# Performance work log

Hardware: AMD Instinct MI355X
Metric: run time of the kernel (lower is better)

The kernel has to match this reference:

```python
import jax, jax.numpy as jnp
import numpy as np

B = 32768
H = 320          # pred_hidden
V = 34           # num_classes
BLANK = V - 1    # padding_idx for embedding


def setup_inputs() -> dict:
    key = jax.random.key(0)
    ks = jax.random.split(key, 12)
    s = 0.05
    embed_W = jax.random.normal(ks[0], (V, H), jnp.float32) * s
    embed_W = embed_W.at[BLANK].set(0.0)  # padding_idx row is zeros in torch
    return {
        "x": jax.random.randint(ks[1], (B,), 0, V, jnp.int32),
        "enc_proj_line": jax.random.normal(ks[2], (B, H), jnp.float32),
        "h": jax.random.normal(ks[3], (1, B, H), jnp.float32),
        "c": jax.random.normal(ks[4], (1, B, H), jnp.float32),
        "embed_W": embed_W,
        "W_ih": jax.random.normal(ks[5], (4 * H, H), jnp.float32) * s,
        "W_hh": jax.random.normal(ks[6], (4 * H, H), jnp.float32) * s,
        "b_ih": jax.random.normal(ks[7], (4 * H,), jnp.float32) * s,
        "b_hh": jax.random.normal(ks[8], (4 * H,), jnp.float32) * s,
        "pred_W": jax.random.normal(ks[9], (H, H), jnp.float32) * s,
        "pred_b": jnp.zeros((H,), jnp.float32),
        "joint_W": jax.random.normal(ks[10], (V, H), jnp.float32) * s,
        "joint_b": jnp.zeros((V,), jnp.float32),
    }


def reference(x, enc_proj_line, h, c, embed_W, W_ih, W_hh, b_ih, b_hh,
              pred_W, pred_b, joint_W, joint_b):
    # embedding lookup: [B, H]
    emb = embed_W[x]
    # single-timestep LSTM cell (torch gate order: i, f, g, o)
    gates = emb @ W_ih.T + b_ih + h[0] @ W_hh.T + b_hh  # [B, 4H]
    i, f, g, o = jnp.split(gates, 4, axis=-1)
    i = jax.nn.sigmoid(i)
    f = jax.nn.sigmoid(f)
    g = jnp.tanh(g)
    o = jax.nn.sigmoid(o)
    c_new = f * c[0] + i * g                 # [B, H]
    h_new = o * jnp.tanh(c_new)              # [B, H] == g[0] (lstm output)
    # pred projection + joint
    pred_proj = h_new @ pred_W.T + pred_b    # [B, H]
    joint_out = (enc_proj_line + pred_proj) @ joint_W.T + joint_b  # [B, V]
    dec = jnp.argmax(joint_out, axis=-1)
    return dec, h_new[None], c_new[None]
```

## Files before the change

kernel.cpp:

```cpp
#include <hip/hip_runtime.h>
#include <math.h>

#define NB 32768
#define H 320
#define V 34
#define N4 1280
#define BM 128
#define BN 128
#define BK 32
#define KSTEPS (H / BK)
#define NWG ((NB / BM) * (N4 / BN))

typedef _Float16 f16;
typedef f16 f16x4 __attribute__((ext_vector_type(4)));
typedef f16 f16x8 __attribute__((ext_vector_type(8)));
typedef float f32x4 __attribute__((ext_vector_type(4)));

#define WS_GTP 0
#define WS_JB2 54400
#define WS_B_BYTE 217744
#define BT_COUNT (N4 * H)
#define WS_JP_BYTE 1856144
#define JP_COUNT (48 * 640)
#define WS_AT_BYTE 1979136
#define AT_COUNT (NB * H)

#define JBM 64
#define JBK 32
#define JKSTEPS 20

#define PREP_P4 1280
#define PREP_P2 50
#define PREP_P0 170
#define PREP_P3 120
#define PREP_NWG (PREP_P4 + PREP_P2 + PREP_P0 + PREP_P3 + 1)

__device__ __forceinline__ float sigf(float x) {
    return 1.0f / (1.0f + __expf(-x));
}
__device__ __forceinline__ float tanh_fast(float x) {
    return 1.0f - 2.0f / (1.0f + __expf(2.0f * x));
}

typedef const __attribute__((address_space(1))) unsigned int* gas_t;
typedef __attribute__((address_space(3))) unsigned int* las_t;

__device__ __forceinline__ void split8(const float* e, f16x8& p1, f16x8& p2) {
    #pragma unroll
    for (int j = 0; j < 8; ++j) {
        f16 a = (f16)e[j];
        p1[j] = a;
        p2[j] = (f16)((e[j] - (float)a) * 2048.0f);
    }
}

__device__ __forceinline__ void split8_res(const float* e, f16x8& p1, f16x8& p2) {
    #pragma unroll
    for (int j = 0; j < 8; ++j) {
        f16 a = (f16)e[j];
        p1[j] = a;
        p2[j] = (f16)(e[j] - (float)a);
    }
}

__global__ void prep(const float* __restrict__ embed_W,
                     const float* __restrict__ W_ih,
                     const float* __restrict__ b_ih,
                     const float* __restrict__ b_hh,
                     const float* __restrict__ pred_W,
                     const float* __restrict__ pred_b,
                     const float* __restrict__ joint_W,
                     const float* __restrict__ joint_b,
                     const float* __restrict__ W_hh,
                     const float* __restrict__ h_in,
                     float* __restrict__ ws) {
    const int bid = blockIdx.x;
    const int t = threadIdx.x;
    if (bid < PREP_P4) {
        int id = bid * 256 + t;
        int ks = id >> 15, m = id & 32767;
        const float* src = h_in + (size_t)m * H + ks * 32;
        f16* at1 = (f16*)((char*)ws + WS_AT_BYTE);
        f16* at2 = at1 + AT_COUNT;
        size_t tbase = ((size_t)(m >> 7) * KSTEPS + ks) * 4096
                       + ((m & 127) >> 4) * 512 + (m & 15) * 8;
        #pragma unroll
        for (int g = 0; g < 4; ++g) {
            float4 v0 = *(const float4*)(src + g * 8);
            float4 v1 = *(const float4*)(src + g * 8 + 4);
            float e[8] = {v0.x, v0.y, v0.z, v0.w, v1.x, v1.y, v1.z, v1.w};
            f16x8 p1, p2;
            split8_res(e, p1, p2);
            *(f16x8*)(at1 + tbase + g * 128) = p1;
            *(f16x8*)(at2 + tbase + g * 128) = p2;
        }
    } else if (bid < PREP_P4 + PREP_P2) {
        int id = (bid - PREP_P4) * 256 + t;
        int ks = id / 1280, n = id - ks * 1280;
        int orig = (n & 3) * H + (n >> 2);
        const float* src = W_hh + (size_t)orig * H + ks * 32;
        f16* bt1 = (f16*)((char*)ws + WS_B_BYTE);
        f16* bt2 = bt1 + BT_COUNT;
        size_t tbase = ((size_t)(n >> 7) * KSTEPS + ks) * 4096
                       + ((n & 127) >> 4) * 512 + (n & 15) * 8;
        #pragma unroll
        for (int g = 0; g < 4; ++g) {
            float4 v0 = *(const float4*)(src + g * 8);
            float4 v1 = *(const float4*)(src + g * 8 + 4);
            float e[8] = {v0.x, v0.y, v0.z, v0.w, v1.x, v1.y, v1.z, v1.w};
            f16x8 p1, p2;
            split8(e, p1, p2);
            *(f16x8*)(bt1 + tbase + g * 128) = p1;
            *(f16x8*)(bt2 + tbase + g * 128) = p2;
        }
    } else if (bid < PREP_P4 + PREP_P2 + PREP_P0) {
        int id = (bid - PREP_P4 - PREP_P2) * 256 + t;
        int v = id / N4, n = id % N4;
        int orig = (n & 3) * H + (n >> 2);
        float acc = b_ih[orig] + b_hh[orig];
        const float* e = embed_W + (size_t)v * H;
        const float* w = W_ih + (size_t)orig * H;
        for (int k = 0; k < H; k += 4) {
            float4 e4 = *(const float4*)(e + k);
            float4 w4 = *(const float4*)(w + k);
            acc = fmaf(e4.x, w4.x, acc);
            acc = fmaf(e4.y, w4.y, acc);
            acc = fmaf(e4.z, w4.z, acc);
            acc = fmaf(e4.w, w4.w, acc);
        }
        ws[WS_GTP + id] = acc;
    } else if (bid < PREP_P4 + PREP_P2 + PREP_P0 + PREP_P3) {
        int id = (bid - PREP_P4 - PREP_P2 - PREP_P0) * 256 + t;
        int n = id / 640, k = id % 640;
        float wv = 0.0f;
        if (n < V) {
            if (k < H) {
                wv = joint_W[(size_t)n * H + k];
            } else {
                float acc = 0.0f;
                const float* jw = joint_W + (size_t)n * H;
                for (int j = 0; j < H; ++j)
                    acc = fmaf(jw[j], pred_W[(size_t)j * H + (k - H)], acc);
                wv = acc;
            }
        }
        f16 w1 = (f16)wv;
        f16 w2 = (f16)((wv - (float)w1) * 2048.0f);
        int kk = k & 31;
        int off = (k >> 5) * 1536 + (n >> 4) * 512 + (kk >> 3) * 128
                  + (n & 15) * 8 + (kk & 7);
        f16* jp1 = (f16*)((char*)ws + WS_JP_BYTE);
        jp1[off] = w1;
        jp1[JP_COUNT + off] = w2;
    } else {
        if (t < V) {
            float acc = joint_b[t];
            const float* jw = joint_W + (size_t)t * H;
            for (int j = 0; j < H; ++j)
                acc = fmaf(jw[j], pred_b[j], acc);
            ws[WS_JB2 + t] = acc;
        }
    }
}

__launch_bounds__(256, 3)
__global__ void lstm_gemm_fast(const int* __restrict__ x,
                               const float* __restrict__ c_in,
                               const float* __restrict__ ws,
                               float* __restrict__ out) {
    __shared__ __align__(16) char smem[32768];
    const int tid = threadIdx.x, lane = tid & 63, w = tid >> 6;

    int l = (blockIdx.x & 7) * (NWG / 8) + (blockIdx.x >> 3);
    const int mb = l / (N4 / BN);
    const int nb = l % (N4 / BN);
    const int m0 = mb * BM, n0 = nb * BN;

    const f16* At1 = (const f16*)((const char*)ws + WS_AT_BYTE);
    const f16* At2 = At1 + AT_COUNT;
    const f16* Bt1 = (const f16*)((const char*)ws + WS_B_BYTE);
    const f16* Bt2 = Bt1 + BT_COUNT;
    const float* gtp = ws + WS_GTP;
    float* hn_out = out + NB;
    float* cn_out = out + NB + (size_t)NB * H;

    const int asub = (w >> 1) * 4;
    const int bsub = (w & 1) * 4;
    const int lo = lane * 8;

    auto stageB = [&](int ks, int parity) {
        const f16* srcp = (w < 2) ? Bt1 : Bt2;
        const f16* src = srcp + (size_t)(nb * KSTEPS + ks) * 4096 + (w & 1) * 2048;
        char* dst = smem + parity * 16384 + (w >> 1) * 8192 + (w & 1) * 4096;
        #pragma unroll
        for (int i = 0; i < 4; ++i) {
            __builtin_amdgcn_global_load_lds(
                (gas_t)(const void*)(src + i * 512 + lane * 8),
                (las_t)(void*)(dst + i * 1024), 16, 0, 0);
        }
    };

    f32x4 acc[4][4];
    #pragma unroll
    for (int i = 0; i < 4; ++i)
        #pragma unroll
        for (int j = 0; j < 4; ++j)
            acc[i][j] = (f32x4){0.f, 0.f, 0.f, 0.f};

    f16x8 a1r[2][4], a2rr[4], b1[4], b2[4];

    stageB(0, 0);
    __builtin_amdgcn_sched_barrier(0);
    {
        const f16* a1b = At1 + (size_t)(mb * KSTEPS + 0) * 4096;
        #pragma unroll
        for (int mi = 0; mi < 4; ++mi)
            a1r[0][mi] = *(const f16x8*)(a1b + (asub + mi) * 512 + lo);
    }
    asm volatile("s_waitcnt vmcnt(4)" ::: "memory");
    __builtin_amdgcn_sched_barrier(0);
    __builtin_amdgcn_s_barrier();

    #pragma unroll
    for (int t = 0; t < KSTEPS; ++t) {
        const int cb = t & 1;
        const f16* B1 = (const f16*)(smem + cb * 16384);
        const f16* B2 = B1 + 4096;

        #pragma unroll
        for (int nj = 0; nj < 4; ++nj)
            b1[nj] = *(const f16x8*)(B1 + (bsub + nj) * 512 + lo);
        #pragma unroll
        for (int nj = 0; nj < 4; ++nj)
            b2[nj] = *(const f16x8*)(B2 + (bsub + nj) * 512 + lo);
        __builtin_amdgcn_sched_barrier(0);
        {
            const f16* a2b = At2 + (size_t)(mb * KSTEPS + t) * 4096;
            #pragma unroll
            for (int mi = 0; mi < 4; ++mi)
                a2rr[mi] = *(const f16x8*)(a2b + (asub + mi) * 512 + lo);
        }
        __builtin_amdgcn_sched_barrier(0);
        if (t < KSTEPS - 1) {
            stageB(t + 1, cb ^ 1);
            __builtin_amdgcn_sched_barrier(0);
            const f16* a1b = At1 + (size_t)(mb * KSTEPS + (t + 1)) * 4096;
            #pragma unroll
            for (int mi = 0; mi < 4; ++mi)
                a1r[cb ^ 1][mi] = *(const f16x8*)(a1b + (asub + mi) * 512 + lo);
            __builtin_amdgcn_sched_barrier(0);
        }

        __builtin_amdgcn_s_setprio(1);
        #pragma unroll
        for (int mi = 0; mi < 4; ++mi)
            #pragma unroll
            for (int nj = 0; nj < 4; ++nj)
                acc[mi][nj] = __builtin_amdgcn_mfma_f32_16x16x32_f16(
                    a1r[cb][mi], b1[nj], acc[mi][nj], 0, 0, 0);
        __builtin_amdgcn_s_setprio(0);
        #pragma unroll
        for (int mi = 0; mi < 4; ++mi)
            #pragma unroll
            for (int j = 0; j < 8; ++j)
                a1r[cb][mi][j] = a1r[cb][mi][j] * (f16)0.00048828125f;
        __builtin_amdgcn_s_setprio(1);
        #pragma unroll
        for (int mi = 0; mi < 4; ++mi)
            #pragma unroll
            for (int nj = 0; nj < 4; ++nj)
                acc[mi][nj] = __builtin_amdgcn_mfma_f32_16x16x32_f16(
                    a1r[cb][mi], b2[nj], acc[mi][nj], 0, 0, 0);
        #pragma unroll
        for (int mi = 0; mi < 4; ++mi)
            #pragma unroll
            for (int nj = 0; nj < 4; ++nj)
                acc[mi][nj] = __builtin_amdgcn_mfma_f32_16x16x32_f16(
                    a2rr[mi], b1[nj], acc[mi][nj], 0, 0, 0);
        __builtin_amdgcn_s_setprio(0);

        if (t < KSTEPS - 1) {
            asm volatile("s_waitcnt vmcnt(4)" ::: "memory");
            __builtin_amdgcn_sched_barrier(0);
            __builtin_amdgcn_s_barrier();
        } else {
            __syncthreads();
        }
    }

    const int wn = (w & 1) * 64;
    const int hk0 = n0 >> 2;
    float* gates = (float*)smem;
    #pragma unroll
    for (int hf = 0; hf < 2; ++hf) {
        if ((w >> 1) == hf) {
            #pragma unroll
            for (int mi = 0; mi < 4; ++mi)
                #pragma unroll
                for (int nj = 0; nj < 4; ++nj) {
                    f32x4 v = acc[mi][nj];
                    int n = wn + nj * 16 + (lane & 15);
                    int lr0 = mi * 16 + (lane >> 4) * 4;
                    #pragma unroll
                    for (int q = 0; q < 4; ++q) {
                        int lr = lr0 + q;
                        gates[lr * 128 + (n ^ ((lr & 7) << 2))] = v[q];
                    }
                }
        }
        __syncthreads();
        #pragma unroll 2
        for (int it = 0; it < 8; ++it) {
            int idx = it * 256 + tid;
            int ml = idx >> 5, hkl = idx & 31;
            int k0 = (ml & 7) << 2;
            f32x4 g4 = *(const f32x4*)&gates[ml * 128 + ((hkl * 4) ^ k0)];
            int m = m0 + hf * 64 + ml;
            int hk = hk0 + hkl;
            int xv = x[m];
            float4 b4 = *(const float4*)(gtp + (size_t)xv * N4 + n0 + hkl * 4);
            float ig = sigf(g4[0] + b4.x);
            float fg = sigf(g4[1] + b4.y);
            float gg = tanh_fast(g4[2] + b4.z);
            float og = sigf(g4[3] + b4.w);
            float cv = c_in[(size_t)m * H + hk];
            float cn = fmaf(fg, cv, ig * gg);
            float hn = og * tanh_fast(cn);
            hn_out[(size_t)m * H + hk] = hn;
            cn_out[(size_t)m * H + hk] = cn;
        }
        if (hf == 0) __syncthreads();
    }
}

__launch_bounds__(256, 2)
__global__ void joint_argmax(const float* __restrict__ enc,
                             const float* __restrict__ ws,
                             float* __restrict__ out) {
    __shared__ __align__(16) char smem[28672];
    const int tid = threadIdx.x, lane = tid & 63, w = tid >> 6;
    const int m0 = blockIdx.x * JBM;

    const f16* Jp1 = (const f16*)((const char*)ws + WS_JP_BYTE);
    const f16* Jp2 = Jp1 + JP_COUNT;
    const float* hn = out + NB;
    const float* jb2 = ws + WS_JB2;

    f16* base = (f16*)smem;

    f32x4 accM[3], accC[3];
    #pragma unroll
    for (int j = 0; j < 3; ++j) {
        accM[j] = (f32x4){0.f, 0.f, 0.f, 0.f};
        accC[j] = (f32x4){0.f, 0.f, 0.f, 0.f};
    }

    auto stage = [&](int t, f16* A1, f16* A2, f16* B1, f16* B2) {
        const float* srcp = (t < 10) ? enc : hn;
        const int koff = (t % 10) * JBK;
        int row = (tid >> 6) * 16 + (tid & 15);
        int k0 = ((tid & 63) >> 4) * 8;
        const float* sp = srcp + (size_t)(m0 + row) * H + koff + k0;
        float4 v0 = *(const float4*)sp;
        float4 v1 = *(const float4*)(sp + 4);
        float e[8] = {v0.x, v0.y, v0.z, v0.w, v1.x, v1.y, v1.z, v1.w};
        f16x8 p1, p2;
        split8(e, p1, p2);
        *(f16x8*)(A1 + tid * 8) = p1;
        *(f16x8*)(A2 + tid * 8) = p2;
        if (tid < 192) {
            *(int4*)(B1 + tid * 8) = *(const int4*)(Jp1 + t * 1536 + tid * 8);
            *(int4*)(B2 + tid * 8) = *(const int4*)(Jp2 + t * 1536 + tid * 8);
        }
    };

    stage(0, base, base + 2048, base + 4096, base + 5632);
    __syncthreads();

    const int lo = lane * 8;
    int cur = 0;
    for (int t = 0; t < JKSTEPS; ++t) {
        if (t < JKSTEPS - 1) {
            f16* nb_ = base + (cur ^ 1) * 7168;
            stage(t + 1, nb_, nb_ + 2048, nb_ + 4096, nb_ + 5632);
        }
        f16* A1 = base + cur * 7168;
        f16* A2 = A1 + 2048;
        f16* B1 = A1 + 4096;
        f16* B2 = A1 + 5632;

        f16x8 a1 = *(const f16x8*)(A1 + w * 512 + lo);
        f16x8 a2 = *(const f16x8*)(A2 + w * 512 + lo);
        f16x8 b1[3], b2[3];
        #pragma unroll
        for (int nj = 0; nj < 3; ++nj) {
            b1[nj] = *(const f16x8*)(B1 + nj * 512 + lo);
            b2[nj] = *(const f16x8*)(B2 + nj * 512 + lo);
        }
        #pragma unroll
        for (int nj = 0; nj < 3; ++nj) {
            accM[nj] = __builtin_amdgcn_mfma_f32_16x16x32_f16(a1, b1[nj], accM[nj], 0, 0, 0);
            accC[nj] = __builtin_amdgcn_mfma_f32_16x16x32_f16(a1, b2[nj], accC[nj], 0, 0, 0);
            accC[nj] = __builtin_amdgcn_mfma_f32_16x16x32_f16(a2, b1[nj], accC[nj], 0, 0, 0);
        }
        __syncthreads();
        cur ^= 1;
    }

    float* lg = (float*)smem;
    const int wm = w * 16;
    #pragma unroll
    for (int nj = 0; nj < 3; ++nj) {
        int n = nj * 16 + (lane & 15);
        int mr = wm + (lane >> 4) * 4;
        #pragma unroll
        for (int q = 0; q < 4; ++q)
            lg[(mr + q) * 49 + n] = fmaf(accC[nj][q], 1.0f / 2048.0f, accM[nj][q]);
    }
    __syncthreads();

    if (tid < JBM) {
        const float* row = lg + tid * 49;
        float best = row[0] + jb2[0];
        int bi = 0;
        #pragma unroll
        for (int v = 1; v < V; ++v) {
            float t2 = row[v] + jb2[v];
            if (t2 > best) { best = t2; bi = v; }
        }
        out[m0 + tid] = (float)bi;
    }
}

extern "C" void kernel_launch(void* const* d_in, const int* in_sizes, int n_in,
                              void* d_out, int out_size, void* d_ws, size_t ws_size,
                              hipStream_t stream) {
    const int*   x       = (const int*)  d_in[0];
    const float* enc     = (const float*)d_in[1];
    const float* h       = (const float*)d_in[2];
    const float* c       = (const float*)d_in[3];
    const float* embed_W = (const float*)d_in[4];
    const float* W_ih    = (const float*)d_in[5];
    const float* W_hh    = (const float*)d_in[6];
    const float* b_ih    = (const float*)d_in[7];
    const float* b_hh    = (const float*)d_in[8];
    const float* pred_W  = (const float*)d_in[9];
    const float* pred_b  = (const float*)d_in[10];
    const float* joint_W = (const float*)d_in[11];
    const float* joint_b = (const float*)d_in[12];
    float* out = (float*)d_out;
    float* ws  = (float*)d_ws;

    prep<<<PREP_NWG, 256, 0, stream>>>(embed_W, W_ih, b_ih, b_hh,
                                       pred_W, pred_b, joint_W, joint_b,
                                       W_hh, h, ws);
    lstm_gemm_fast<<<NWG, 256, 0, stream>>>(x, c, ws, out);
    joint_argmax<<<NB / JBM, 256, 0, stream>>>(enc, ws, out);
}
```

Baseline: 165.3 us.

## Stage two K-steps per LDS window and prefetch cell state before GEMM

The LSTM gate GEMM now stages B tiles two K-steps at a time into a 64 KB double-buffered LDS window, which halves the number of block barriers. A operands are loaded directly per half-window rather than through a register double buffer. The c_in values are prefetched into registers before the main loop, and the epilogue writes all gates to LDS in one pass instead of two halves. The cost is double the LDS and the occupancy hint dropping from 3 to 2 blocks per CU, with less explicit overlap of A loads.

```diff
diff --git a/kernel.cpp b/kernel.cpp
--- a/kernel.cpp
+++ b/kernel.cpp
@@ -7,8 +7,8 @@
 #define N4 1280
 #define BM 128
 #define BN 128
-#define BK 32
-#define KSTEPS (H / BK)
+#define KSTEPS 10
+#define NWIN 5
 #define NWG ((NB / BM) * (N4 / BN))
 
 typedef _Float16 f16;
@@ -163,12 +163,12 @@
     }
 }
 
-__launch_bounds__(256, 3)
+__launch_bounds__(256, 2)
 __global__ void lstm_gemm_fast(const int* __restrict__ x,
                                const float* __restrict__ c_in,
                                const float* __restrict__ ws,
                                float* __restrict__ out) {
-    __shared__ __align__(16) char smem[32768];
+    __shared__ __align__(16) char smem[65536];
     const int tid = threadIdx.x, lane = tid & 63, w = tid >> 6;
 
     int l = (blockIdx.x & 7) * (NWG / 8) + (blockIdx.x >> 3);
@@ -188,15 +188,21 @@
     const int bsub = (w & 1) * 4;
     const int lo = lane * 8;
 
-    auto stageB = [&](int ks, int parity) {
+    auto stageB = [&](int T, int parity) {
         const f16* srcp = (w < 2) ? Bt1 : Bt2;
-        const f16* src = srcp + (size_t)(nb * KSTEPS + ks) * 4096 + (w & 1) * 2048;
-        char* dst = smem + parity * 16384 + (w >> 1) * 8192 + (w & 1) * 4096;
-        #pragma unroll
-        for (int i = 0; i < 4; ++i) {
-            __builtin_amdgcn_global_load_lds(
-                (gas_t)(const void*)(src + i * 512 + lane * 8),
-                (las_t)(void*)(dst + i * 1024), 16, 0, 0);
+        const int p = (w < 2) ? 0 : 1;
+        #pragma unroll
+        for (int ksl = 0; ksl < 2; ++ksl) {
+            const f16* src = srcp + (size_t)(nb * KSTEPS + 2 * T + ksl) * 4096
+                             + (w & 1) * 2048;
+            char* dst = smem + parity * 32768 + p * 16384 + ksl * 8192
+                        + (w & 1) * 4096;
+            #pragma unroll
+            for (int i = 0; i < 4; ++i) {
+                __builtin_amdgcn_global_load_lds(
+                    (gas_t)(const void*)(src + i * 512 + lane * 8),
+                    (las_t)(void*)(dst + i * 1024), 16, 0, 0);
+            }
         }
     };
 
@@ -207,49 +213,38 @@
         for (int j = 0; j < 4; ++j)
             acc[i][j] = (f32x4){0.f, 0.f, 0.f, 0.f};
 
-    f16x8 a1r[2][4], a2rr[4], b1[4], b2[4];
-
     stageB(0, 0);
-    __builtin_amdgcn_sched_barrier(0);
-    {
-        const f16* a1b = At1 + (size_t)(mb * KSTEPS + 0) * 4096;
-        #pragma unroll
-        for (int mi = 0; mi < 4; ++mi)
-            a1r[0][mi] = *(const f16x8*)(a1b + (asub + mi) * 512 + lo);
-    }
-    asm volatile("s_waitcnt vmcnt(4)" ::: "memory");
-    __builtin_amdgcn_sched_barrier(0);
-    __builtin_amdgcn_s_barrier();
-
-    #pragma unroll
-    for (int t = 0; t < KSTEPS; ++t) {
-        const int cb = t & 1;
-        const f16* B1 = (const f16*)(smem + cb * 16384);
-        const f16* B2 = B1 + 4096;
-
-        #pragma unroll
-        for (int nj = 0; nj < 4; ++nj)
-            b1[nj] = *(const f16x8*)(B1 + (bsub + nj) * 512 + lo);
-        #pragma unroll
-        for (int nj = 0; nj < 4; ++nj)
-            b2[nj] = *(const f16x8*)(B2 + (bsub + nj) * 512 + lo);
-        __builtin_amdgcn_sched_barrier(0);
+    __syncthreads();
+
+    const int hk0 = n0 >> 2;
+    float cpre[16];
+    #pragma unroll
+    for (int it = 0; it < 16; ++it)
+        cpre[it] = c_in[(size_t)(m0 + it * 8 + (tid >> 5)) * H + hk0 + (tid & 31)];
+
+    #pragma unroll
+    for (int T = 0; T < NWIN; ++T) {
+        const int par = T & 1;
+        const f16* B1 = (const f16*)(smem + par * 32768);
+        const f16* B2 = B1 + 8192;
+
+        f16x8 b1a[4], b2a[4];
+        #pragma unroll
+        for (int nj = 0; nj < 4; ++nj) {
+            b1a[nj] = *(const f16x8*)(B1 + (bsub + nj) * 512 + lo);
+            b2a[nj] = *(const f16x8*)(B2 + (bsub + nj) * 512 + lo);
+        }
+        f16x8 a1a[4], a2a[4];
         {
-            const f16* a2b = At2 + (size_t)(mb * KSTEPS + t) * 4096;
-            #pragma unroll
-            for (int mi = 0; mi < 4; ++mi)
-                a2rr[mi] = *(const f16x8*)(a2b + (asub + mi) * 512 + lo);
-        }
-        __builtin_amdgcn_sched_barrier(0);
-        if (t < KSTEPS - 1) {
-            stageB(t + 1, cb ^ 1);
-            __builtin_amdgcn_sched_barrier(0);
-            const f16* a1b = At1 + (size_t)(mb * KSTEPS + (t + 1)) * 4096;
-            #pragma unroll
-            for (int mi = 0; mi < 4; ++mi)
-                a1r[cb ^ 1][mi] = *(const f16x8*)(a1b + (asub + mi) * 512 + lo);
-            __builtin_amdgcn_sched_barrier(0);
-        }
+            const f16* a1b = At1 + (size_t)(mb * KSTEPS + 2 * T) * 4096;
+            const f16* a2b = At2 + (size_t)(mb * KSTEPS + 2 * T) * 4096;
+            #pragma unroll
+            for (int mi = 0; mi < 4; ++mi) {
+                a1a[mi] = *(const f16x8*)(a1b + (asub + mi) * 512 + lo);
+                a2a[mi] = *(const f16x8*)(a2b + (asub + mi) * 512 + lo);
+            }
+        }
+        if (T < NWIN - 1) stageB(T + 1, par ^ 1);
 
         __builtin_amdgcn_s_setprio(1);
         #pragma unroll
@@ -257,79 +252,113 @@
             #pragma unroll
             for (int nj = 0; nj < 4; ++nj)
                 acc[mi][nj] = __builtin_amdgcn_mfma_f32_16x16x32_f16(
-                    a1r[cb][mi], b1[nj], acc[mi][nj], 0, 0, 0);
+                    a1a[mi], b1a[nj], acc[mi][nj], 0, 0, 0);
         __builtin_amdgcn_s_setprio(0);
         #pragma unroll
         for (int mi = 0; mi < 4; ++mi)
             #pragma unroll
             for (int j = 0; j < 8; ++j)
-                a1r[cb][mi][j] = a1r[cb][mi][j] * (f16)0.00048828125f;
+                a1a[mi][j] = a1a[mi][j] * (f16)0.00048828125f;
         __builtin_amdgcn_s_setprio(1);
         #pragma unroll
         for (int mi = 0; mi < 4; ++mi)
             #pragma unroll
             for (int nj = 0; nj < 4; ++nj)
                 acc[mi][nj] = __builtin_amdgcn_mfma_f32_16x16x32_f16(
-                    a1r[cb][mi], b2[nj], acc[mi][nj], 0, 0, 0);
-        #pragma unroll
-        for (int mi = 0; mi < 4; ++mi)
-            #pragma unroll
-            for (int nj = 0; nj < 4; ++nj)
-                acc[mi][nj] = __builtin_amdgcn_mfma_f32_16x16x32_f16(
-                    a2rr[mi], b1[nj], acc[mi][nj], 0, 0, 0);
+                    a1a[mi], b2a[nj], acc[mi][nj], 0, 0, 0);
         __builtin_amdgcn_s_setprio(0);
 
-        if (t < KSTEPS - 1) {
-            asm volatile("s_waitcnt vmcnt(4)" ::: "memory");
-            __builtin_amdgcn_sched_barrier(0);
-            __builtin_amdgcn_s_barrier();
-        } else {
-            __syncthreads();
-        }
-    }
-
-    const int wn = (w & 1) * 64;
-    const int hk0 = n0 >> 2;
+        f16x8 a1c[4], a2c[4];
+        {
+            const f16* a1b = At1 + (size_t)(mb * KSTEPS + 2 * T + 1) * 4096;
+            const f16* a2b = At2 + (size_t)(mb * KSTEPS + 2 * T + 1) * 4096;
+            #pragma unroll
+            for (int mi = 0; mi < 4; ++mi) {
+                a1c[mi] = *(const f16x8*)(a1b + (asub + mi) * 512 + lo);
+                a2c[mi] = *(const f16x8*)(a2b + (asub + mi) * 512 + lo);
+            }
+        }
+
+        __builtin_amdgcn_s_setprio(1);
+        #pragma unroll
+        for (int mi = 0; mi < 4; ++mi)
+            #pragma unroll
+            for (int nj = 0; nj < 4; ++nj)
+                acc[mi][nj] = __builtin_amdgcn_mfma_f32_16x16x32_f16(
+                    a2a[mi], b1a[nj], acc[mi][nj], 0, 0, 0);
+        __builtin_amdgcn_s_setprio(0);
+
+        f16x8 b1c[4], b2c[4];
+        #pragma unroll
+        for (int nj = 0; nj < 4; ++nj) {
+            b1c[nj] = *(const f16x8*)(B1 + 4096 + (bsub + nj) * 512 + lo);
+            b2c[nj] = *(const f16x8*)(B2 + 4096 + (bsub + nj) * 512 + lo);
+        }
+        __builtin_amdgcn_s_setprio(1);
+        #pragma unroll
+        for (int mi = 0; mi < 4; ++mi)
+            #pragma unroll
+            for (int nj = 0; nj < 4; ++nj)
+                acc[mi][nj] = __builtin_amdgcn_mfma_f32_16x16x32_f16(
+                    a1c[mi], b1c[nj], acc[mi][nj], 0, 0, 0);
+        __builtin_amdgcn_s_setprio(0);
+        #pragma unroll
+        for (int mi = 0; mi < 4; ++mi)
+            #pragma unroll
+            for (int j = 0; j < 8; ++j)
+                a1c[mi][j] = a1c[mi][j] * (f16)0.00048828125f;
+        __builtin_amdgcn_s_setprio(1);
+        #pragma unroll
+        for (int mi = 0; mi < 4; ++mi)
+            #pragma unroll
+            for (int nj = 0; nj < 4; ++nj)
+                acc[mi][nj] = __builtin_amdgcn_mfma_f32_16x16x32_f16(
+                    a1c[mi], b2c[nj], acc[mi][nj], 0, 0, 0);
+        #pragma unroll
+        for (int mi = 0; mi < 4; ++mi)
+            #pragma unroll
+            for (int nj = 0; nj < 4; ++nj)
+                acc[mi][nj] = __builtin_amdgcn_mfma_f32_16x16x32_f16(
+                    a2c[mi], b1c[nj], acc[mi][nj], 0, 0, 0);
+        __builtin_amdgcn_s_setprio(0);
+
+        __syncthreads();
+    }
+
+    const int wm = (w >> 1) * 64, wn = (w & 1) * 64;
     float* gates = (float*)smem;
     #pragma unroll
-    for (int hf = 0; hf < 2; ++hf) {
-        if ((w >> 1) == hf) {
-            #pragma unroll
-            for (int mi = 0; mi < 4; ++mi)
-                #pragma unroll
-                for (int nj = 0; nj < 4; ++nj) {
-                    f32x4 v = acc[mi][nj];
-                    int n = wn + nj * 16 + (lane & 15);
-                    int lr0 = mi * 16 + (lane >> 4) * 4;
-                    #pragma unroll
-                    for (int q = 0; q < 4; ++q) {
-                        int lr = lr0 + q;
-                        gates[lr * 128 + (n ^ ((lr & 7) << 2))] = v[q];
-                    }
-                }
-        }
-        __syncthreads();
-        #pragma unroll 2
-        for (int it = 0; it < 8; ++it) {
-            int idx = it * 256 + tid;
-            int ml = idx >> 5, hkl = idx & 31;
-            int k0 = (ml & 7) << 2;
-            f32x4 g4 = *(const f32x4*)&gates[ml * 128 + ((hkl * 4) ^ k0)];
-            int m = m0 + hf * 64 + ml;
-            int hk = hk0 + hkl;
-            int xv = x[m];
-            float4 b4 = *(const float4*)(gtp + (size_t)xv * N4 + n0 + hkl * 4);
-            float ig = sigf(g4[0] + b4.x);
-            float fg = sigf(g4[1] + b4.y);
-            float gg = tanh_fast(g4[2] + b4.z);
-            float og = sigf(g4[3] + b4.w);
-            float cv = c_in[(size_t)m * H + hk];
-            float cn = fmaf(fg, cv, ig * gg);
-            float hn = og * tanh_fast(cn);
-            hn_out[(size_t)m * H + hk] = hn;
-            cn_out[(size_t)m * H + hk] = cn;
-        }
-        if (hf == 0) __syncthreads();
+    for (int mi = 0; mi < 4; ++mi)
+        #pragma unroll
+        for (int nj = 0; nj < 4; ++nj) {
+            f32x4 v = acc[mi][nj];
+            int n = wn + nj * 16 + (lane & 15);
+            int r0 = wm + mi * 16 + (lane >> 4) * 4;
+            #pragma unroll
+            for (int q = 0; q < 4; ++q) {
+                int row = r0 + q;
+                gates[row * 128 + (n ^ ((row & 7) << 2))] = v[q];
+            }
+        }
+    __syncthreads();
+
+    #pragma unroll
+    for (int it = 0; it < 16; ++it) {
+        int ml = it * 8 + (tid >> 5), hkl = tid & 31;
+        int k0s = (ml & 7) << 2;
+        f32x4 g4 = *(const f32x4*)&gates[ml * 128 + ((hkl * 4) ^ k0s)];
+        int m = m0 + ml;
+        int hk = hk0 + hkl;
+        int xv = x[m];
+        float4 b4 = *(const float4*)(gtp + (size_t)xv * N4 + n0 + hkl * 4);
+        float ig = sigf(g4[0] + b4.x);
+        float fg = sigf(g4[1] + b4.y);
+        float gg = tanh_fast(g4[2] + b4.z);
+        float og = sigf(g4[3] + b4.w);
+        float cn = fmaf(fg, cpre[it], ig * gg);
+        float hn = og * tanh_fast(cn);
+        hn_out[(size_t)m * H + hk] = hn;
+        cn_out[(size_t)m * H + hk] = cn;
     }
 }
 
```

Result: faster. 159.6 us (median of 3 runs) (-3.4%).

## Use 512-thread blocks with 2x4 wave grid and prefetch c_in before GEMM

Applied to the files above, without the earlier changes.

Doubles the LSTM GEMM workgroup to 8 waves, each computing a 64x32 sub-tile instead of 64x64, which halves the accumulator registers and raises the occupancy bound. The B staging and A register double-buffering are reorganised so that the next k-step's A fragments load between MFMA groups. The c_in values are prefetched into registers before the main loop, and the x/bias loads in the epilogue are batched, so the epilogue's global latency overlaps with compute. The cost is more waves per barrier and a different vmcnt accounting that must stay correct.

```diff
diff --git a/kernel.cpp b/kernel.cpp
--- a/kernel.cpp
+++ b/kernel.cpp
@@ -7,8 +7,7 @@
 #define N4 1280
 #define BM 128
 #define BN 128
-#define BK 32
-#define KSTEPS (H / BK)
+#define KSTEPS 10
 #define NWG ((NB / BM) * (N4 / BN))
 
 typedef _Float16 f16;
@@ -163,7 +162,7 @@
     }
 }
 
-__launch_bounds__(256, 3)
+__launch_bounds__(512, 4)
 __global__ void lstm_gemm_fast(const int* __restrict__ x,
                                const float* __restrict__ c_in,
                                const float* __restrict__ ws,
@@ -184,103 +183,115 @@
     float* hn_out = out + NB;
     float* cn_out = out + NB + (size_t)NB * H;
 
-    const int asub = (w >> 1) * 4;
-    const int bsub = (w & 1) * 4;
+    const int wr = w >> 2;
+    const int wc = w & 3;
+    const int asub = wr * 4;
+    const int bsub = wc * 2;
     const int lo = lane * 8;
 
     auto stageB = [&](int ks, int parity) {
-        const f16* srcp = (w < 2) ? Bt1 : Bt2;
-        const f16* src = srcp + (size_t)(nb * KSTEPS + ks) * 4096 + (w & 1) * 2048;
-        char* dst = smem + parity * 16384 + (w >> 1) * 8192 + (w & 1) * 4096;
-        #pragma unroll
-        for (int i = 0; i < 4; ++i) {
+        const f16* srcp = (w < 4) ? Bt1 : Bt2;
+        const f16* src = srcp + (size_t)(nb * KSTEPS + ks) * 4096 + (w & 3) * 1024;
+        char* dst = smem + parity * 16384 + ((w < 4) ? 0 : 8192) + (w & 3) * 2048;
+        #pragma unroll
+        for (int i = 0; i < 2; ++i) {
             __builtin_amdgcn_global_load_lds(
                 (gas_t)(const void*)(src + i * 512 + lane * 8),
                 (las_t)(void*)(dst + i * 1024), 16, 0, 0);
         }
     };
 
-    f32x4 acc[4][4];
-    #pragma unroll
-    for (int i = 0; i < 4; ++i)
-        #pragma unroll
-        for (int j = 0; j < 4; ++j)
-            acc[i][j] = (f32x4){0.f, 0.f, 0.f, 0.f};
-
-    f16x8 a1r[2][4], a2rr[4], b1[4], b2[4];
+    f32x4 acc[4][2];
+    #pragma unroll
+    for (int i = 0; i < 4; ++i) {
+        acc[i][0] = (f32x4){0.f, 0.f, 0.f, 0.f};
+        acc[i][1] = (f32x4){0.f, 0.f, 0.f, 0.f};
+    }
+
+    f16x8 a1r[4], a2r[4];
 
     stageB(0, 0);
     __builtin_amdgcn_sched_barrier(0);
     {
-        const f16* a1b = At1 + (size_t)(mb * KSTEPS + 0) * 4096;
-        #pragma unroll
-        for (int mi = 0; mi < 4; ++mi)
-            a1r[0][mi] = *(const f16x8*)(a1b + (asub + mi) * 512 + lo);
-    }
-    asm volatile("s_waitcnt vmcnt(4)" ::: "memory");
+        const f16* a1b = At1 + (size_t)(mb * KSTEPS) * 4096;
+        const f16* a2b = At2 + (size_t)(mb * KSTEPS) * 4096;
+        #pragma unroll
+        for (int mi = 0; mi < 4; ++mi) {
+            a1r[mi] = *(const f16x8*)(a1b + (asub + mi) * 512 + lo);
+            a2r[mi] = *(const f16x8*)(a2b + (asub + mi) * 512 + lo);
+        }
+    }
+    __builtin_amdgcn_sched_barrier(0);
+    const int hk0 = n0 >> 2;
+    float cpre[8];
+    #pragma unroll
+    for (int j = 0; j < 8; ++j)
+        cpre[j] = c_in[(size_t)(m0 + j * 16 + (tid >> 5)) * H + hk0 + (tid & 31)];
+    __builtin_amdgcn_sched_barrier(0);
+    asm volatile("s_waitcnt vmcnt(16)" ::: "memory");
     __builtin_amdgcn_sched_barrier(0);
     __builtin_amdgcn_s_barrier();
 
     #pragma unroll
     for (int t = 0; t < KSTEPS; ++t) {
-        const int cb = t & 1;
-        const f16* B1 = (const f16*)(smem + cb * 16384);
+        const int par = t & 1;
+        if (t < KSTEPS - 1) {
+            stageB(t + 1, par ^ 1);
+            __builtin_amdgcn_sched_barrier(0);
+        }
+        const f16* B1 = (const f16*)(smem + par * 16384);
         const f16* B2 = B1 + 4096;
 
-        #pragma unroll
-        for (int nj = 0; nj < 4; ++nj)
+        f16x8 b1[2], b2[2];
+        #pragma unroll
+        for (int nj = 0; nj < 2; ++nj) {
             b1[nj] = *(const f16x8*)(B1 + (bsub + nj) * 512 + lo);
-        #pragma unroll
-        for (int nj = 0; nj < 4; ++nj)
             b2[nj] = *(const f16x8*)(B2 + (bsub + nj) * 512 + lo);
-        __builtin_amdgcn_sched_barrier(0);
-        {
-            const f16* a2b = At2 + (size_t)(mb * KSTEPS + t) * 4096;
+        }
+
+        __builtin_amdgcn_s_setprio(1);
+        #pragma unroll
+        for (int mi = 0; mi < 4; ++mi)
+            #pragma unroll
+            for (int nj = 0; nj < 2; ++nj)
+                acc[mi][nj] = __builtin_amdgcn_mfma_f32_16x16x32_f16(
+                    a1r[mi], b1[nj], acc[mi][nj], 0, 0, 0);
+        __builtin_amdgcn_s_setprio(0);
+        #pragma unroll
+        for (int mi = 0; mi < 4; ++mi)
+            #pragma unroll
+            for (int j = 0; j < 8; ++j)
+                a1r[mi][j] = a1r[mi][j] * (f16)0.00048828125f;
+        __builtin_amdgcn_s_setprio(1);
+        #pragma unroll
+        for (int mi = 0; mi < 4; ++mi)
+            #pragma unroll
+            for (int nj = 0; nj < 2; ++nj)
+                acc[mi][nj] = __builtin_amdgcn_mfma_f32_16x16x32_f16(
+                    a1r[mi], b2[nj], acc[mi][nj], 0, 0, 0);
+        __builtin_amdgcn_s_setprio(0);
+        if (t < KSTEPS - 1) {
+            const f16* a1b = At1 + (size_t)(mb * KSTEPS + t + 1) * 4096;
             #pragma unroll
             for (int mi = 0; mi < 4; ++mi)
-                a2rr[mi] = *(const f16x8*)(a2b + (asub + mi) * 512 + lo);
-        }
-        __builtin_amdgcn_sched_barrier(0);
+                a1r[mi] = *(const f16x8*)(a1b + (asub + mi) * 512 + lo);
+            __builtin_amdgcn_sched_barrier(0);
+        }
+        __builtin_amdgcn_s_setprio(1);
+        #pragma unroll
+        for (int mi = 0; mi < 4; ++mi)
+            #pragma unroll
+            for (int nj = 0; nj < 2; ++nj)
+                acc[mi][nj] = __builtin_amdgcn_mfma_f32_16x16x32_f16(
+                    a2r[mi], b1[nj], acc[mi][nj], 0, 0, 0);
+        __builtin_amdgcn_s_setprio(0);
         if (t < KSTEPS - 1) {
-            stageB(t + 1, cb ^ 1);
+            const f16* a2b = At2 + (size_t)(mb * KSTEPS + t + 1) * 4096;
+            #pragma unroll
+            for (int mi = 0; mi < 4; ++mi)
+                a2r[mi] = *(const f16x8*)(a2b + (asub + mi) * 512 + lo);
             __builtin_amdgcn_sched_barrier(0);
-            const f16* a1b = At1 + (size_t)(mb * KSTEPS + (t + 1)) * 4096;
-            #pragma unroll
-            for (int mi = 0; mi < 4; ++mi)
-                a1r[cb ^ 1][mi] = *(const f16x8*)(a1b + (asub + mi) * 512 + lo);
-            __builtin_amdgcn_sched_barrier(0);
-        }
-
-        __builtin_amdgcn_s_setprio(1);
-        #pragma unroll
-        for (int mi = 0; mi < 4; ++mi)
-            #pragma unroll
-            for (int nj = 0; nj < 4; ++nj)
-                acc[mi][nj] = __builtin_amdgcn_mfma_f32_16x16x32_f16(
-                    a1r[cb][mi], b1[nj], acc[mi][nj], 0, 0, 0);
-        __builtin_amdgcn_s_setprio(0);
-        #pragma unroll
-        for (int mi = 0; mi < 4; ++mi)
-            #pragma unroll
-            for (int j = 0; j < 8; ++j)
-                a1r[cb][mi][j] = a1r[cb][mi][j] * (f16)0.00048828125f;
-        __builtin_amdgcn_s_setprio(1);
-        #pragma unroll
-        for (int mi = 0; mi < 4; ++mi)
-            #pragma unroll
-            for (int nj = 0; nj < 4; ++nj)
-                acc[mi][nj] = __builtin_amdgcn_mfma_f32_16x16x32_f16(
-                    a1r[cb][mi], b2[nj], acc[mi][nj], 0, 0, 0);
-        #pragma unroll
-        for (int mi = 0; mi < 4; ++mi)
-            #pragma unroll
-            for (int nj = 0; nj < 4; ++nj)
-                acc[mi][nj] = __builtin_amdgcn_mfma_f32_16x16x32_f16(
-                    a2rr[mi], b1[nj], acc[mi][nj], 0, 0, 0);
-        __builtin_amdgcn_s_setprio(0);
-
-        if (t < KSTEPS - 1) {
-            asm volatile("s_waitcnt vmcnt(4)" ::: "memory");
+            asm volatile("s_waitcnt vmcnt(8)" ::: "memory");
             __builtin_amdgcn_sched_barrier(0);
             __builtin_amdgcn_s_barrier();
         } else {
@@ -288,18 +299,16 @@
         }
     }
 
-    const int wn = (w & 1) * 64;
-    const int hk0 = n0 >> 2;
     float* gates = (float*)smem;
     #pragma unroll
     for (int hf = 0; hf < 2; ++hf) {
-        if ((w >> 1) == hf) {
+        if (wr == hf) {
             #pragma unroll
             for (int mi = 0; mi < 4; ++mi)
                 #pragma unroll
-                for (int nj = 0; nj < 4; ++nj) {
+                for (int nj = 0; nj < 2; ++nj) {
                     f32x4 v = acc[mi][nj];
-                    int n = wn + nj * 16 + (lane & 15);
+                    int n = wc * 32 + nj * 16 + (lane & 15);
                     int lr0 = mi * 16 + (lane >> 4) * 4;
                     #pragma unroll
                     for (int q = 0; q < 4; ++q) {
@@ -309,22 +318,26 @@
                 }
         }
         __syncthreads();
-        #pragma unroll 2
-        for (int it = 0; it < 8; ++it) {
-            int idx = it * 256 + tid;
-            int ml = idx >> 5, hkl = idx & 31;
-            int k0 = (ml & 7) << 2;
-            f32x4 g4 = *(const f32x4*)&gates[ml * 128 + ((hkl * 4) ^ k0)];
+        int xv[4];
+        #pragma unroll
+        for (int it = 0; it < 4; ++it)
+            xv[it] = x[m0 + hf * 64 + it * 16 + (tid >> 5)];
+        float4 b4[4];
+        #pragma unroll
+        for (int it = 0; it < 4; ++it)
+            b4[it] = *(const float4*)(gtp + (size_t)xv[it] * N4 + n0 + (tid & 31) * 4);
+        #pragma unroll
+        for (int it = 0; it < 4; ++it) {
+            int ml = it * 16 + (tid >> 5), hkl = tid & 31;
+            int k0s = (ml & 7) << 2;
+            f32x4 g4 = *(const f32x4*)&gates[ml * 128 + ((hkl * 4) ^ k0s)];
             int m = m0 + hf * 64 + ml;
             int hk = hk0 + hkl;
-            int xv = x[m];
-            float4 b4 = *(const float4*)(gtp + (size_t)xv * N4 + n0 + hkl * 4);
-            float ig = sigf(g4[0] + b4.x);
-            float fg = sigf(g4[1] + b4.y);
-            float gg = tanh_fast(g4[2] + b4.z);
-            float og = sigf(g4[3] + b4.w);
-            float cv = c_in[(size_t)m * H + hk];
-            float cn = fmaf(fg, cv, ig * gg);
+            float ig = sigf(g4[0] + b4[it].x);
+            float fg = sigf(g4[1] + b4[it].y);
+            float gg = tanh_fast(g4[2] + b4[it].z);
+            float og = sigf(g4[3] + b4[it].w);
+            float cn = fmaf(fg, cpre[hf * 4 + it], ig * gg);
             float hn = og * tanh_fast(cn);
             hn_out[(size_t)m * H + hk] = hn;
             cn_out[(size_t)m * H + hk] = cn;
@@ -454,6 +467,6 @@
     prep<<<PREP_NWG, 256, 0, stream>>>(embed_W, W_ih, b_ih, b_hh,
                                        pred_W, pred_b, joint_W, joint_b,
                                        W_hh, h, ws);
-    lstm_gemm_fast<<<NWG, 256, 0, stream>>>(x, c, ws, out);
+    lstm_gemm_fast<<<NWG, 512, 0, stream>>>(x, c, ws, out);
     joint_argmax<<<NB / JBM, 256, 0, stream>>>(enc, ws, out);
 }
```

Result: slower. 170.7 us (+3.3%).
